# Performance work log

Hardware: AMD Instinct MI355X
Metric: run time of the kernel (lower is better)

The kernel has to match this reference:

```python
import jax, jax.numpy as jnp
import numpy as np

B, G = 256, 24
N = B * G
D_IN, HEADS, D_HEAD = 128, 8, 64  # out_channels = in_channels//2 = 64, concat=False
EFF = HEADS * D_HEAD
EPS = 1e-5
SCALE = float(np.sqrt(D_HEAD))

def _gelu(x):
    return jax.nn.gelu(x, approximate=False)

def _pff(x, w1, b1, w2, b2):
    # PositionwiseFeedForward, dropout=0 (eval)
    return _gelu(x @ w1.T + b1) @ w2.T + b2

def _graph_norm_global(x, w, b, ms):
    # GraphNorm called without batch -> single graph over all N nodes
    mean = jnp.mean(x, axis=0, keepdims=True)
    out = x - mean * ms
    var = jnp.mean(out * out, axis=0, keepdims=True)
    return w * out / jnp.sqrt(var + EPS) + b

def _graph_norm(x, w, b, ms, batch, nseg):
    cnt = jax.ops.segment_sum(jnp.ones((x.shape[0],), x.dtype), batch, nseg)[:, None]
    mean = jax.ops.segment_sum(x, batch, nseg) / cnt
    out = x - mean[batch] * ms
    var = jax.ops.segment_sum(out * out, batch, nseg) / cnt
    return w * out / jnp.sqrt(var + EPS)[batch] + b

def _segment_softmax(logits, seg, nseg):
    m = jax.ops.segment_max(logits, seg, num_segments=nseg)
    e = jnp.exp(logits - m[seg])
    s = jax.ops.segment_sum(e, seg, num_segments=nseg)
    return e / (s[seg] + 1e-16)

def _attn_conv(x, edge_index, p):
    (nq_w, nq_b, nq_ms, wq, bq, wk, bk, wv, bv,
     no_w, no_b, no_ms, o_w1, o_b1, o_w2, o_b2) = p
    n = x.shape[0]
    xin = x
    xn = _graph_norm_global(x, nq_w, nq_b, nq_ms)
    q = (xn @ wq.T + bq).reshape(n, HEADS, D_HEAD)
    k = (xn @ wk.T + bk).reshape(n, HEADS, D_HEAD)
    v = (xn @ wv.T + bv).reshape(n, HEADS, D_HEAD)
    loops = jnp.arange(n, dtype=edge_index.dtype)  # add_self_loops appends
    src = jnp.concatenate([edge_index[0], loops])
    dst = jnp.concatenate([edge_index[1], loops])
    qk = jnp.sum(q[dst] * k[src], axis=-1) / SCALE          # [E', H]
    alpha = _segment_softmax(qk, dst, n)                     # segment softmax over dst
    aggr = jax.ops.segment_sum(v[src] * alpha[:, :, None], dst, num_segments=n)  # [N,H,Dh]
    aggr = aggr.mean(axis=1)                                 # concat=False: head mean -> [N,64]
    init = xin.reshape(n, D_IN // D_HEAD, D_HEAD).sum(axis=1)  # sum-fold 128 -> 64 residual
    h = aggr + init
    hn = _graph_norm_global(h, no_w, no_b, no_ms)
    return h + _pff(hn, o_w1, o_b1, o_w2, o_b2)


def setup_inputs() -> dict:
    key = jax.random.key(0)
    ks = jax.random.split(key, 12)
    # block-dense edges: fully connected within each set, no self loops
    a = np.arange(G)
    ii, jj = np.meshgrid(a, a, indexing='ij')
    m = ii != jj
    dst_l, src_l = ii[m], jj[m]
    offs = (np.arange(B) * G)[:, None]
    src = (src_l[None, :] + offs).reshape(-1)
    dst = (dst_l[None, :] + offs).reshape(-1)
    edge_index = jnp.asarray(np.stack([src, dst]), dtype=jnp.int64)
    batch = jnp.asarray(np.repeat(np.arange(B), G), dtype=jnp.int64)
    ptr = jnp.asarray(np.arange(B + 1) * G, dtype=jnp.int64)
    x = jax.random.normal(ks[0], (N, D_IN), jnp.float32)
    def lin(k, o, i):
        return jax.random.normal(k, (o, i), jnp.float32) * (1.0 / np.sqrt(i))
    d = dict(x=x, edge_index=edge_index, ptr=ptr, batch=batch)
    d.update(nq_w=jnp.ones((D_IN,)), nq_b=jnp.zeros((D_IN,)), nq_ms=jnp.ones((D_IN,)))
    d.update(wq=lin(ks[1], EFF, D_IN), bq=jnp.zeros((EFF,)),
             wk=lin(ks[2], EFF, D_IN), bk=jnp.zeros((EFF,)),
             wv=lin(ks[3], EFF, D_IN), bv=jnp.zeros((EFF,)))
    d.update(no_w=jnp.ones((D_HEAD,)), no_b=jnp.zeros((D_HEAD,)), no_ms=jnp.ones((D_HEAD,)))
    d.update(o_w1=lin(ks[4], D_HEAD, D_HEAD), o_b1=jnp.zeros((D_HEAD,)),
             o_w2=lin(ks[5], D_HEAD, D_HEAD), o_b2=jnp.zeros((D_HEAD,)))
    d.update(pn_w=jnp.ones((D_HEAD,)), pn_b=jnp.zeros((D_HEAD,)), pn_ms=jnp.ones((D_HEAD,)))
    d.update(p_w1=lin(ks[6], D_HEAD, D_HEAD), p_b1=jnp.zeros((D_HEAD,)),
             p_w2=lin(ks[7], 1, D_HEAD), p_b2=jnp.zeros((1,)))
    return d


def reference(x, edge_index, ptr, batch,
              nq_w, nq_b, nq_ms, wq, bq, wk, bk, wv, bv,
              no_w, no_b, no_ms, o_w1, o_b1, o_w2, o_b2,
              pn_w, pn_b, pn_ms, p_w1, p_b1, p_w2, p_b2):
    nseg = ptr.shape[0] - 1
    h = _attn_conv(x, edge_index,
                   (nq_w, nq_b, nq_ms, wq, bq, wk, bk, wv, bv,
                    no_w, no_b, no_ms, o_w1, o_b1, o_w2, o_b2))   # [N,64]
    hn = _graph_norm(h, pn_w, pn_b, pn_ms, batch, nseg)
    score = _pff(hn, p_w1, p_b1, p_w2, p_b2)                       # [N,1]
    w = _segment_softmax(score[:, 0], batch, nseg)[:, None]        # per-set softmax
    return jax.ops.segment_sum(x * w, batch, num_segments=nseg)    # [B, 128]
```

## Files before the change

kernel.cpp:

```cpp
#include <hip/hip_runtime.h>
#include <stdint.h>


#define N_NODES 6144
#define GSIZE 24
#define NGRAPH 256
#define DIN 128
#define DH 64
#define EFF 512
#define EPSN 1e-5f

typedef __attribute__((ext_vector_type(8))) __bf16 bf16x8;
typedef __attribute__((ext_vector_type(4))) float f32x4;
union U16B { uint4 u; bf16x8 v; unsigned short s[8]; };

__device__ inline unsigned short f2bf(float f){
  unsigned u = __float_as_uint(f);
  u += 0x7fff + ((u>>16)&1);
  return (unsigned short)(u>>16);
}
__device__ inline float gelu_exact(float x){ return 0.5f*x*(1.0f+erff(x*0.70710678118654752f)); }

#define XS    0
#define HS    256
#define WT1   81920
#define WT2   86016
#define PWT1  90112
#define FBo   94208
#define WCVT_BYTE  385024
#define HCOMB_BYTE 778240

#define QSTRIDE 516

__global__ __launch_bounds__(256)
void k_pre(const float* __restrict__ x,
           const float* __restrict__ o_w1, const float* __restrict__ o_w2,
           const float* __restrict__ p_w1,
           const float* __restrict__ o_b1, const float* __restrict__ o_b2,
           const float* __restrict__ p_b1, const float* __restrict__ p_w2,
           const float* __restrict__ p_b2,
           const float* __restrict__ wq, const float* __restrict__ wk,
           const float* __restrict__ wv,
           float* __restrict__ wsf){
  int t = threadIdx.x;
  int bi = blockIdx.x;
  if(bi < 192){
    int c = t & 127, h = t >> 7;
    float s = 0.f, q = 0.f;
    #pragma unroll
    for(int r = 0; r < 16; ++r){
      float v = x[(size_t)(bi*32 + h + 2*r)*DIN + c];
      s += v; q += v*v;
    }
    __shared__ float sm[256], sm2[256];
    sm[t] = s; sm2[t] = q;
    __syncthreads();
    if(t < 128){
      atomicAdd(&wsf[XS + t],       sm[t] + sm[t+128]);
      atomicAdd(&wsf[XS + 128 + t], sm2[t] + sm2[t+128]);
    }
    return;
  }
  if(bi < 195){
    const float* src; float* dst;
    if(bi == 192){ src = o_w1; dst = wsf + WT1; }
    else if(bi == 193){ src = o_w2; dst = wsf + WT2; }
    else { src = p_w1; dst = wsf + PWT1; }
    for(int p = t; p < DH*DH; p += 256){
      int r = p >> 6, c = p & 63;
      dst[c*DH + r] = src[p];
    }
    if(bi == 192){
      float* fb = wsf + FBo;
      if(t < 64){
        fb[t]       = o_b1[t];
        fb[64 + t]  = o_b2[t];
        fb[128 + t] = p_b1[t];
        fb[192 + t] = p_w2[t];
      }
      if(t == 0) fb[256] = p_b2[0];
    }
    return;
  }
  int j = bi - 195;
  int mat = j >> 2, seg = j & 3;
  const float* src = (mat==0) ? wq : (mat==1) ? wk : wv;
  unsigned short* dst = (unsigned short*)((char*)wsf + WCVT_BYTE)
                        + (size_t)mat*EFF*DIN + seg*16384;
  const float* sp = src + seg*16384;
  for(int e = t*8; e < 16384; e += 2048){
    float4 a = *(const float4*)(sp + e);
    float4 b = *(const float4*)(sp + e + 4);
    U16B o;
    o.s[0]=f2bf(a.x); o.s[1]=f2bf(a.y); o.s[2]=f2bf(a.z); o.s[3]=f2bf(a.w);
    o.s[4]=f2bf(b.x); o.s[5]=f2bf(b.y); o.s[6]=f2bf(b.z); o.s[7]=f2bf(b.w);
    *(uint4*)(dst + e) = o.u;
  }
}

#define LOADW(nt, W, B) do{ \
  const int mat_ = (nt)>>2, sub_ = (nt)&3; \
  const unsigned short* wp_ = wcvt + (size_t)mat_*EFF*DIN \
      + (size_t)(h*64 + sub_*16 + m)*DIN + lq*8; \
  W[0] = *(const uint4*)(wp_);      W[1] = *(const uint4*)(wp_ + 32); \
  W[2] = *(const uint4*)(wp_ + 64); W[3] = *(const uint4*)(wp_ + 96); \
  const float* bias_ = (mat_==0) ? bq : (mat_==1) ? bk : bv; \
  B = *(const float4*)(bias_ + h*64 + sub_*16 + lq*4); \
}while(0)

#define COMPW(nt, W, B) do{ \
  const int mat_ = (nt)>>2, sub_ = (nt)&3; \
  f32x4 a0_ = {0.f,0.f,0.f,0.f}, a1_ = {0.f,0.f,0.f,0.f}; \
  U16B w8_; \
  w8_.u = W[0]; \
  a0_ = __builtin_amdgcn_mfma_f32_16x16x32_bf16(w8_.v, afr[0][0], a0_, 0, 0, 0); \
  a1_ = __builtin_amdgcn_mfma_f32_16x16x32_bf16(w8_.v, afr[1][0], a1_, 0, 0, 0); \
  w8_.u = W[1]; \
  a0_ = __builtin_amdgcn_mfma_f32_16x16x32_bf16(w8_.v, afr[0][1], a0_, 0, 0, 0); \
  a1_ = __builtin_amdgcn_mfma_f32_16x16x32_bf16(w8_.v, afr[1][1], a1_, 0, 0, 0); \
  w8_.u = W[2]; \
  a0_ = __builtin_amdgcn_mfma_f32_16x16x32_bf16(w8_.v, afr[0][2], a0_, 0, 0, 0); \
  a1_ = __builtin_amdgcn_mfma_f32_16x16x32_bf16(w8_.v, afr[1][2], a1_, 0, 0, 0); \
  w8_.u = W[3]; \
  a0_ = __builtin_amdgcn_mfma_f32_16x16x32_bf16(w8_.v, afr[0][3], a0_, 0, 0, 0); \
  a1_ = __builtin_amdgcn_mfma_f32_16x16x32_bf16(w8_.v, afr[1][3], a1_, 0, 0, 0); \
  float* dst_ = qlds + mat_*(GSIZE*QSTRIDE); \
  const int col_ = h*64 + sub_*16 + lq*4; \
  { float4 o_; o_.x=a0_[0]+B.x; o_.y=a0_[1]+B.y; o_.z=a0_[2]+B.z; o_.w=a0_[3]+B.w; \
    *(float4*)(dst_ + m*QSTRIDE + col_) = o_; } \
  if(m < 8){ float4 o_; o_.x=a1_[0]+B.x; o_.y=a1_[1]+B.y; o_.z=a1_[2]+B.z; o_.w=a1_[3]+B.w; \
    *(float4*)(dst_ + (16+m)*QSTRIDE + col_) = o_; } \
}while(0)

__global__ __launch_bounds__(512)
void k_attn2(const float* __restrict__ x,
             const float* __restrict__ bq, const float* __restrict__ bk,
             const float* __restrict__ bv,
             const float* __restrict__ nq_w, const float* __restrict__ nq_b,
             const float* __restrict__ nq_ms,
             float* __restrict__ ws, float* __restrict__ hcomb){
  __shared__ __align__(16) float qlds[3*GSIZE*QSTRIDE];
  __shared__ __align__(16) float hv[GSIZE][68];
  __shared__ float A1s[DIN], C1s[DIN];

  int t = threadIdx.x, g = blockIdx.x, base = g*GSIZE;
  int h = t >> 6, l = t & 63;
  const unsigned short* wcvt = (const unsigned short*)((const char*)ws + WCVT_BYTE);

  for(int i = t; i < GSIZE*68; i += 512) ((float*)hv)[i] = 0.f;

  if(t < 128){
    float s1 = ws[XS + t];
    float q1 = ws[XS + 128 + t];
    float mean = s1 * (1.0f / N_NODES);
    float ex2  = q1 * (1.0f / N_NODES);
    float cm   = mean * nq_ms[t];
    float var  = ex2 - 2.f*cm*mean + cm*cm;
    float rstd = rsqrtf(var + EPSN);
    float a    = nq_w[t] * rstd;
    A1s[t] = a; C1s[t] = nq_b[t] - a*cm;
  }
  __syncthreads();

  int m = l & 15, lq = l >> 4;

  bf16x8 afr[2][4];
  #pragma unroll
  for(int mt = 0; mt < 2; ++mt){
    int row = mt*16 + m; if(row > GSIZE-1) row = GSIZE-1;
    const float* xr = x + (size_t)(base + row)*DIN;
    #pragma unroll
    for(int kk = 0; kk < 4; ++kk){
      int k0 = kk*32 + lq*8;
      float4 a = *(const float4*)(xr + k0);
      float4 b = *(const float4*)(xr + k0 + 4);
      U16B u;
      u.s[0] = f2bf(a.x*A1s[k0+0] + C1s[k0+0]);
      u.s[1] = f2bf(a.y*A1s[k0+1] + C1s[k0+1]);
      u.s[2] = f2bf(a.z*A1s[k0+2] + C1s[k0+2]);
      u.s[3] = f2bf(a.w*A1s[k0+3] + C1s[k0+3]);
      u.s[4] = f2bf(b.x*A1s[k0+4] + C1s[k0+4]);
      u.s[5] = f2bf(b.y*A1s[k0+5] + C1s[k0+5]);
      u.s[6] = f2bf(b.z*A1s[k0+6] + C1s[k0+6]);
      u.s[7] = f2bf(b.w*A1s[k0+7] + C1s[k0+7]);
      afr[mt][kk] = u.v;
    }
  }

  {
    uint4 wA[4], wB[4], wC[4];
    float4 bA, bB, bC;
    LOADW(0, wA, bA);  LOADW(1, wB, bB);
    LOADW(2, wC, bC);  COMPW(0, wA, bA);
    LOADW(3, wA, bA);  COMPW(1, wB, bB);
    LOADW(4, wB, bB);  COMPW(2, wC, bC);
    LOADW(5, wC, bC);  COMPW(3, wA, bA);
    LOADW(6, wA, bA);  COMPW(4, wB, bB);
    LOADW(7, wB, bB);  COMPW(5, wC, bC);
    LOADW(8, wC, bC);  COMPW(6, wA, bA);
    LOADW(9, wA, bA);  COMPW(7, wB, bB);
    LOADW(10, wB, bB); COMPW(8, wC, bC);
    LOADW(11, wC, bC); COMPW(9, wA, bA);
    COMPW(10, wB, bB);
    COMPW(11, wC, bC);
  }

  {
    int r0 = 3*(l >> 3), j0 = 3*(l & 7);
    const float* qp = qlds + r0*QSTRIDE + h*64;
    const float* kp = qlds + GSIZE*QSTRIDE + j0*QSTRIDE + h*64;
    float s00=0.f,s01=0.f,s02=0.f,s10=0.f,s11=0.f,s12=0.f,s20=0.f,s21=0.f,s22=0.f;
    #pragma unroll
    for(int d4 = 0; d4 < 16; ++d4){
      float4 q0 = *(const float4*)(qp + d4*4);
      float4 q1 = *(const float4*)(qp + QSTRIDE + d4*4);
      float4 q2 = *(const float4*)(qp + 2*QSTRIDE + d4*4);
      float4 k0 = *(const float4*)(kp + d4*4);
      float4 k1 = *(const float4*)(kp + QSTRIDE + d4*4);
      float4 k2 = *(const float4*)(kp + 2*QSTRIDE + d4*4);
      s00 += q0.x*k0.x + q0.y*k0.y + q0.z*k0.z + q0.w*k0.w;
      s01 += q0.x*k1.x + q0.y*k1.y + q0.z*k1.z + q0.w*k1.w;
      s02 += q0.x*k2.x + q0.y*k2.y + q0.z*k2.z + q0.w*k2.w;
      s10 += q1.x*k0.x + q1.y*k0.y + q1.z*k0.z + q1.w*k0.w;
      s11 += q1.x*k1.x + q1.y*k1.y + q1.z*k1.z + q1.w*k1.w;
      s12 += q1.x*k2.x + q1.y*k2.y + q1.z*k2.z + q1.w*k2.w;
      s20 += q2.x*k0.x + q2.y*k0.y + q2.z*k0.z + q2.w*k0.w;
      s21 += q2.x*k1.x + q2.y*k1.y + q2.z*k1.z + q2.w*k1.w;
      s22 += q2.x*k2.x + q2.y*k2.y + q2.z*k2.z + q2.w*k2.w;
    }
    float a0, a1, a2, m0, su, inv;
    float* STb = qlds + h*64;
    a0 = s00*0.125f; a1 = s01*0.125f; a2 = s02*0.125f;
    m0 = fmaxf(fmaxf(a0, a1), a2);
    #pragma unroll
    for(int o = 1; o < 8; o <<= 1) m0 = fmaxf(m0, __shfl_xor(m0, o, 8));
    a0 = __expf(a0-m0); a1 = __expf(a1-m0); a2 = __expf(a2-m0);
    su = a0 + a1 + a2;
    #pragma unroll
    for(int o = 1; o < 8; o <<= 1) su += __shfl_xor(su, o, 8);
    inv = 1.0f/(su + 1e-16f);
    STb[(j0+0)*QSTRIDE + r0] = a0*inv; STb[(j0+1)*QSTRIDE + r0] = a1*inv; STb[(j0+2)*QSTRIDE + r0] = a2*inv;
    a0 = s10*0.125f; a1 = s11*0.125f; a2 = s12*0.125f;
    m0 = fmaxf(fmaxf(a0, a1), a2);
    #pragma unroll
    for(int o = 1; o < 8; o <<= 1) m0 = fmaxf(m0, __shfl_xor(m0, o, 8));
    a0 = __expf(a0-m0); a1 = __expf(a1-m0); a2 = __expf(a2-m0);
    su = a0 + a1 + a2;
    #pragma unroll
    for(int o = 1; o < 8; o <<= 1) su += __shfl_xor(su, o, 8);
    inv = 1.0f/(su + 1e-16f);
    STb[(j0+0)*QSTRIDE + r0+1] = a0*inv; STb[(j0+1)*QSTRIDE + r0+1] = a1*inv; STb[(j0+2)*QSTRIDE + r0+1] = a2*inv;
    a0 = s20*0.125f; a1 = s21*0.125f; a2 = s22*0.125f;
    m0 = fmaxf(fmaxf(a0, a1), a2);
    #pragma unroll
    for(int o = 1; o < 8; o <<= 1) m0 = fmaxf(m0, __shfl_xor(m0, o, 8));
    a0 = __expf(a0-m0); a1 = __expf(a1-m0); a2 = __expf(a2-m0);
    su = a0 + a1 + a2;
    #pragma unroll
    for(int o = 1; o < 8; o <<= 1) su += __shfl_xor(su, o, 8);
    inv = 1.0f/(su + 1e-16f);
    STb[(j0+0)*QSTRIDE + r0+2] = a0*inv; STb[(j0+1)*QSTRIDE + r0+2] = a1*inv; STb[(j0+2)*QSTRIDE + r0+2] = a2*inv;
  }

  {
    float o24[GSIZE];
    #pragma unroll
    for(int r = 0; r < GSIZE; ++r) o24[r] = 0.f;
    const float* vp  = qlds + 2*GSIZE*QSTRIDE + h*64 + l;
    const float* STb = qlds + h*64;
    #pragma unroll
    for(int j = 0; j < GSIZE; ++j){
      float v = vp[j*QSTRIDE];
      #pragma unroll
      for(int rq = 0; rq < 6; ++rq){
        float4 p4 = *(const float4*)(STb + j*QSTRIDE + rq*4);
        o24[rq*4+0] = fmaf(p4.x, v, o24[rq*4+0]);
        o24[rq*4+1] = fmaf(p4.y, v, o24[rq*4+1]);
        o24[rq*4+2] = fmaf(p4.z, v, o24[rq*4+2]);
        o24[rq*4+3] = fmaf(p4.w, v, o24[rq*4+3]);
      }
    }
    #pragma unroll
    for(int r = 0; r < GSIZE; ++r) atomicAdd(&hv[r][l], o24[r]);
  }
  __syncthreads();

  #pragma unroll
  for(int sl = 0; sl < 3; ++sl){
    int idx = t + sl*512;
    int r = idx >> 6, d = idx & 63;
    const float* xr = x + (size_t)(base + r)*DIN;
    float hval = hv[r][d]*0.125f + xr[d] + xr[64 + d];
    hcomb[(size_t)(base + r)*DH + d] = hval;
    hv[r][d] = hval;
  }
  __syncthreads();
  if(t < 64){
    float s1 = 0.f, s2 = 0.f;
    #pragma unroll
    for(int i = 0; i < GSIZE; ++i){ float v = hv[i][t]; s1 += v; s2 += v*v; }
    atomicAdd(&ws[HS + t],      s1);
    atomicAdd(&ws[HS + 64 + t], s2);
  }
}

__global__ __launch_bounds__(512)
void k_final(const float* __restrict__ x,
             const float* __restrict__ hbuf, const float* __restrict__ ws,
             const float* __restrict__ no_w, const float* __restrict__ no_b,
             const float* __restrict__ no_ms,
             const float* __restrict__ pn_w, const float* __restrict__ pn_b,
             const float* __restrict__ pn_ms,
             float* __restrict__ out){
  __shared__ __align__(16) float W1[4096];
  __shared__ __align__(16) float W2[4096];
  __shared__ __align__(16) float PW1[4096];
  __shared__ __align__(16) float fbs[260];
  __shared__ __align__(16) float hs[GSIZE][68];
  __shared__ __align__(16) float hn[GSIZE][68];
  __shared__ __align__(16) float ts[GSIZE][68];
  __shared__ float A2s[DH], C2s[DH];
  __shared__ float a3[DH], c3[DH];
  __shared__ float scores[GSIZE], wsm[GSIZE];

  int t = threadIdx.x;
  int base = blockIdx.x * GSIZE;
  int c = t & 63, i0 = t >> 6;

  {
    const float4* s1 = (const float4*)(ws + WT1);
    const float4* s2 = (const float4*)(ws + WT2);
    const float4* s3 = (const float4*)(ws + PWT1);
    #pragma unroll
    for(int it = 0; it < 2; ++it){
      int i = t + it*512;
      ((float4*)W1)[i]  = s1[i];
      ((float4*)W2)[i]  = s2[i];
      ((float4*)PW1)[i] = s3[i];
    }
    if(t < 257) fbs[t] = ws[FBo + t];
    if(t < DH){
      float a1 = ws[HS + t];
      float a2 = ws[HS + 64 + t];
      float mean = a1 * (1.0f / N_NODES);
      float ex2  = a2 * (1.0f / N_NODES);
      float cm   = mean * no_ms[t];
      float var  = ex2 - 2.f*cm*mean + cm*cm;
      float rstd = rsqrtf(var + EPSN);
      float a    = no_w[t] * rstd;
      A2s[t] = a; C2s[t] = no_b[t] - a*cm;
    }
  }
  __syncthreads();
  {
    float a2 = A2s[c];
    float c2 = C2s[c];
    #pragma unroll
    for(int r = 0; r < 3; ++r){
      int i = i0 + 8*r;
      float hvv = hbuf[(size_t)(base + i)*DH + c];
      hs[i][c] = hvv;
      hn[i][c] = a2*hvv + c2;
    }
  }
  __syncthreads();

  {
    float acc[3];
    #pragma unroll
    for(int r = 0; r < 3; ++r) acc[r] = fbs[c];
    #pragma unroll 16
    for(int k = 0; k < DH; ++k){
      float w = W1[k*DH + c];
      #pragma unroll
      for(int r = 0; r < 3; ++r) acc[r] = fmaf(hn[i0 + 8*r][k], w, acc[r]);
    }
    #pragma unroll
    for(int r = 0; r < 3; ++r) ts[i0 + 8*r][c] = gelu_exact(acc[r]);
  }
  __syncthreads();

  {
    float acc[3];
    #pragma unroll
    for(int r = 0; r < 3; ++r) acc[r] = fbs[64 + c];
    #pragma unroll 16
    for(int k = 0; k < DH; ++k){
      float w = W2[k*DH + c];
      #pragma unroll
      for(int r = 0; r < 3; ++r) acc[r] = fmaf(ts[i0 + 8*r][k], w, acc[r]);
    }
    #pragma unroll
    for(int r = 0; r < 3; ++r) hs[i0 + 8*r][c] += acc[r];
  }
  __syncthreads();

  if(t < DH){
    float s1 = 0.f, s2 = 0.f;
    #pragma unroll
    for(int i = 0; i < GSIZE; i++){ float v = hs[i][t]; s1 += v; s2 += v*v; }
    float mean = s1 * (1.0f / GSIZE);
    float ex2  = s2 * (1.0f / GSIZE);
    float cm   = mean * pn_ms[t];
    float var  = ex2 - 2.f*cm*mean + cm*cm;
    float rstd = rsqrtf(var + EPSN);
    float a    = pn_w[t] * rstd;
    a3[t] = a; c3[t] = pn_b[t] - a*cm;
  }
  __syncthreads();

  {
    float acc[3];
    #pragma unroll
    for(int r = 0; r < 3; ++r) acc[r] = fbs[128 + c];
    #pragma unroll 16
    for(int k = 0; k < DH; ++k){
      float w  = PW1[k*DH + c];
      float ak = a3[k], ck = c3[k];
      #pragma unroll
      for(int r = 0; r < 3; ++r){
        float hnv = fmaf(ak, hs[i0 + 8*r][k], ck);
        acc[r] = fmaf(hnv, w, acc[r]);
      }
    }
    #pragma unroll
    for(int r = 0; r < 3; ++r) ts[i0 + 8*r][c] = gelu_exact(acc[r]);
  }
  __syncthreads();

  if(t < GSIZE){
    const float4* tp = (const float4*)ts[t];
    const float4* wp = (const float4*)(fbs + 192);
    float s = fbs[256];
    #pragma unroll
    for(int q = 0; q < 16; ++q){
      float4 a = tp[q], b = wp[q];
      s += a.x*b.x + a.y*b.y + a.z*b.z + a.w*b.w;
    }
    scores[t] = s;
  }
  __syncthreads();
  if(t < GSIZE){
    float mx = -1e30f;
    #pragma unroll
    for(int j = 0; j < GSIZE; j++) mx = fmaxf(mx, scores[j]);
    float sum = 0.f;
    #pragma unroll
    for(int j = 0; j < GSIZE; j++) sum += __expf(scores[j] - mx);
    wsm[t] = __expf(scores[t] - mx) / (sum + 1e-16f);
  }
  __syncthreads();
  if(t < DIN){
    float s = 0.f;
    #pragma unroll 8
    for(int i = 0; i < GSIZE; i++) s += wsm[i] * x[(size_t)(base+i)*DIN + t];
    out[(size_t)blockIdx.x*DIN + t] = s;
  }
}

extern "C" void kernel_launch(void* const* d_in, const int* in_sizes, int n_in,
                              void* d_out, int out_size, void* d_ws, size_t ws_size,
                              hipStream_t stream){
  (void)in_sizes; (void)n_in; (void)out_size; (void)ws_size;
  const float* x    = (const float*)d_in[0];
  const float* nq_w = (const float*)d_in[4];
  const float* nq_b = (const float*)d_in[5];
  const float* nq_ms= (const float*)d_in[6];
  const float* wq   = (const float*)d_in[7];
  const float* bq   = (const float*)d_in[8];
  const float* wk   = (const float*)d_in[9];
  const float* bk   = (const float*)d_in[10];
  const float* wv   = (const float*)d_in[11];
  const float* bv   = (const float*)d_in[12];
  const float* no_w = (const float*)d_in[13];
  const float* no_b = (const float*)d_in[14];
  const float* no_ms= (const float*)d_in[15];
  const float* o_w1 = (const float*)d_in[16];
  const float* o_b1 = (const float*)d_in[17];
  const float* o_w2 = (const float*)d_in[18];
  const float* o_b2 = (const float*)d_in[19];
  const float* pn_w = (const float*)d_in[20];
  const float* pn_b = (const float*)d_in[21];
  const float* pn_ms= (const float*)d_in[22];
  const float* p_w1 = (const float*)d_in[23];
  const float* p_b1 = (const float*)d_in[24];
  const float* p_w2 = (const float*)d_in[25];
  const float* p_b2 = (const float*)d_in[26];

  float* ws    = (float*)d_ws;
  float* hcomb = (float*)((char*)d_ws + HCOMB_BYTE);

  hipMemsetAsync(d_ws, 0, 384*sizeof(float), stream);
  k_pre<<<207, 256, 0, stream>>>(x, o_w1, o_w2, p_w1, o_b1, o_b2, p_b1, p_w2, p_b2,
                                 wq, wk, wv, ws);
  k_attn2<<<NGRAPH, 512, 0, stream>>>(x, bq, bk, bv, nq_w, nq_b, nq_ms, ws, hcomb);
  k_final<<<NGRAPH, 512, 0, stream>>>(x, hcomb, ws, no_w, no_b, no_ms,
                                      pn_w, pn_b, pn_ms, (float*)d_out);
}
```

Baseline: 167.0 us.

## Split attention across two blocks per graph by head halves, add residual fixup kernel

The attention kernel now launches two blocks per graph, each handling four heads, with two waves per head splitting the QKV output tiles, the dot-product dimension and the output rows. Partial head sums go into a zeroed hcomb buffer through global atomics. A new small kernel then adds the folded input residual and accumulates the GraphNorm statistics. The aim is more parallelism and smaller per-block shared memory, at the cost of an extra launch, a larger memset, global atomics and more block barriers.

Result: slower. 176.1 us (+5.4%).

```diff
diff --git a/kernel.cpp b/kernel.cpp
--- a/kernel.cpp
+++ b/kernel.cpp
@@ -23,14 +23,14 @@
 
 #define XS    0
 #define HS    256
-#define WT1   81920
-#define WT2   86016
-#define PWT1  90112
-#define FBo   94208
-#define WCVT_BYTE  385024
-#define HCOMB_BYTE 778240
-
-#define QSTRIDE 516
+#define HCF   384
+#define WT1   393600
+#define WT2   397696
+#define PWT1  401792
+#define FBo   405888
+#define WCVT_BYTE  1703936
+
+#define QS3 260
 
 __global__ __launch_bounds__(256)
 void k_pre(const float* __restrict__ x,
@@ -98,17 +98,17 @@
   }
 }
 
-#define LOADW(nt, W, B) do{ \
+#define LOADW3(nt, W, B) do{ \
   const int mat_ = (nt)>>2, sub_ = (nt)&3; \
   const unsigned short* wp_ = wcvt + (size_t)mat_*EFF*DIN \
-      + (size_t)(h*64 + sub_*16 + m)*DIN + lq*8; \
+      + (size_t)(gh*64 + sub_*16 + m)*DIN + lq*8; \
   W[0] = *(const uint4*)(wp_);      W[1] = *(const uint4*)(wp_ + 32); \
   W[2] = *(const uint4*)(wp_ + 64); W[3] = *(const uint4*)(wp_ + 96); \
   const float* bias_ = (mat_==0) ? bq : (mat_==1) ? bk : bv; \
-  B = *(const float4*)(bias_ + h*64 + sub_*16 + lq*4); \
+  B = *(const float4*)(bias_ + gh*64 + sub_*16 + lq*4); \
 }while(0)
 
-#define COMPW(nt, W, B) do{ \
+#define COMPW3(nt, W, B) do{ \
   const int mat_ = (nt)>>2, sub_ = (nt)&3; \
   f32x4 a0_ = {0.f,0.f,0.f,0.f}, a1_ = {0.f,0.f,0.f,0.f}; \
   U16B w8_; \
@@ -124,30 +124,34 @@
   w8_.u = W[3]; \
   a0_ = __builtin_amdgcn_mfma_f32_16x16x32_bf16(w8_.v, afr[0][3], a0_, 0, 0, 0); \
   a1_ = __builtin_amdgcn_mfma_f32_16x16x32_bf16(w8_.v, afr[1][3], a1_, 0, 0, 0); \
-  float* dst_ = qlds + mat_*(GSIZE*QSTRIDE); \
-  const int col_ = h*64 + sub_*16 + lq*4; \
+  float* dst_ = qlds + mat_*(GSIZE*QS3); \
+  const int col_ = hh*64 + sub_*16 + lq*4; \
   { float4 o_; o_.x=a0_[0]+B.x; o_.y=a0_[1]+B.y; o_.z=a0_[2]+B.z; o_.w=a0_[3]+B.w; \
-    *(float4*)(dst_ + m*QSTRIDE + col_) = o_; } \
+    *(float4*)(dst_ + m*QS3 + col_) = o_; } \
   if(m < 8){ float4 o_; o_.x=a1_[0]+B.x; o_.y=a1_[1]+B.y; o_.z=a1_[2]+B.z; o_.w=a1_[3]+B.w; \
-    *(float4*)(dst_ + (16+m)*QSTRIDE + col_) = o_; } \
+    *(float4*)(dst_ + (16+m)*QS3 + col_) = o_; } \
 }while(0)
 
 __global__ __launch_bounds__(512)
-void k_attn2(const float* __restrict__ x,
+void k_attn3(const float* __restrict__ x,
              const float* __restrict__ bq, const float* __restrict__ bk,
              const float* __restrict__ bv,
              const float* __restrict__ nq_w, const float* __restrict__ nq_b,
              const float* __restrict__ nq_ms,
              float* __restrict__ ws, float* __restrict__ hcomb){
-  __shared__ __align__(16) float qlds[3*GSIZE*QSTRIDE];
-  __shared__ __align__(16) float hv[GSIZE][68];
-  __shared__ float A1s[DIN], C1s[DIN];
-
-  int t = threadIdx.x, g = blockIdx.x, base = g*GSIZE;
-  int h = t >> 6, l = t & 63;
+  __shared__ __align__(16) float qlds[3*GSIZE*QS3];
+  __shared__ __align__(16) float hv[GSIZE][DH];
+  float* A1s = qlds;
+  float* C1s = qlds + 128;
+
+  int t = threadIdx.x, b = blockIdx.x;
+  int base = (b >> 1)*GSIZE;
+  int w = t >> 6, l = t & 63;
+  int hh = w >> 1, half = w & 1;
+  int gh = (b & 1)*4 + hh;
   const unsigned short* wcvt = (const unsigned short*)((const char*)ws + WCVT_BYTE);
 
-  for(int i = t; i < GSIZE*68; i += 512) ((float*)hv)[i] = 0.f;
+  for(int i = t; i < GSIZE*DH; i += 512) ((float*)hv)[i] = 0.f;
 
   if(t < 128){
     float s1 = ws[XS + t];
@@ -186,38 +190,36 @@
       afr[mt][kk] = u.v;
     }
   }
+  __syncthreads();
 
   {
     uint4 wA[4], wB[4], wC[4];
     float4 bA, bB, bC;
-    LOADW(0, wA, bA);  LOADW(1, wB, bB);
-    LOADW(2, wC, bC);  COMPW(0, wA, bA);
-    LOADW(3, wA, bA);  COMPW(1, wB, bB);
-    LOADW(4, wB, bB);  COMPW(2, wC, bC);
-    LOADW(5, wC, bC);  COMPW(3, wA, bA);
-    LOADW(6, wA, bA);  COMPW(4, wB, bB);
-    LOADW(7, wB, bB);  COMPW(5, wC, bC);
-    LOADW(8, wC, bC);  COMPW(6, wA, bA);
-    LOADW(9, wA, bA);  COMPW(7, wB, bB);
-    LOADW(10, wB, bB); COMPW(8, wC, bC);
-    LOADW(11, wC, bC); COMPW(9, wA, bA);
-    COMPW(10, wB, bB);
-    COMPW(11, wC, bC);
-  }
-
-  {
-    int r0 = 3*(l >> 3), j0 = 3*(l & 7);
-    const float* qp = qlds + r0*QSTRIDE + h*64;
-    const float* kp = qlds + GSIZE*QSTRIDE + j0*QSTRIDE + h*64;
-    float s00=0.f,s01=0.f,s02=0.f,s10=0.f,s11=0.f,s12=0.f,s20=0.f,s21=0.f,s22=0.f;
-    #pragma unroll
-    for(int d4 = 0; d4 < 16; ++d4){
+    int nb = half*6;
+    LOADW3(nb+0, wA, bA);  LOADW3(nb+1, wB, bB);
+    LOADW3(nb+2, wC, bC);  COMPW3(nb+0, wA, bA);
+    LOADW3(nb+3, wA, bA);  COMPW3(nb+1, wB, bB);
+    LOADW3(nb+4, wB, bB);  COMPW3(nb+2, wC, bC);
+    LOADW3(nb+5, wC, bC);  COMPW3(nb+3, wA, bA);
+    COMPW3(nb+4, wB, bB);
+    COMPW3(nb+5, wC, bC);
+  }
+  __syncthreads();
+
+  int r0 = half*12 + 3*(l >> 4), j0 = 3*(l & 7);
+  float s00=0.f,s01=0.f,s02=0.f,s10=0.f,s11=0.f,s12=0.f,s20=0.f,s21=0.f,s22=0.f;
+  {
+    int d8 = (l >> 3) & 1;
+    const float* qp = qlds + r0*QS3 + hh*64 + d8*32;
+    const float* kp = qlds + GSIZE*QS3 + j0*QS3 + hh*64 + d8*32;
+    #pragma unroll
+    for(int d4 = 0; d4 < 8; ++d4){
       float4 q0 = *(const float4*)(qp + d4*4);
-      float4 q1 = *(const float4*)(qp + QSTRIDE + d4*4);
-      float4 q2 = *(const float4*)(qp + 2*QSTRIDE + d4*4);
+      float4 q1 = *(const float4*)(qp + QS3 + d4*4);
+      float4 q2 = *(const float4*)(qp + 2*QS3 + d4*4);
       float4 k0 = *(const float4*)(kp + d4*4);
-      float4 k1 = *(const float4*)(kp + QSTRIDE + d4*4);
-      float4 k2 = *(const float4*)(kp + 2*QSTRIDE + d4*4);
+      float4 k1 = *(const float4*)(kp + QS3 + d4*4);
+      float4 k2 = *(const float4*)(kp + 2*QS3 + d4*4);
       s00 += q0.x*k0.x + q0.y*k0.y + q0.z*k0.z + q0.w*k0.w;
       s01 += q0.x*k1.x + q0.y*k1.y + q0.z*k1.z + q0.w*k1.w;
       s02 += q0.x*k2.x + q0.y*k2.y + q0.z*k2.z + q0.w*k2.w;
@@ -228,8 +230,15 @@
       s21 += q2.x*k1.x + q2.y*k1.y + q2.z*k1.z + q2.w*k1.w;
       s22 += q2.x*k2.x + q2.y*k2.y + q2.z*k2.z + q2.w*k2.w;
     }
+    s00 += __shfl_xor(s00, 8); s01 += __shfl_xor(s01, 8); s02 += __shfl_xor(s02, 8);
+    s10 += __shfl_xor(s10, 8); s11 += __shfl_xor(s11, 8); s12 += __shfl_xor(s12, 8);
+    s20 += __shfl_xor(s20, 8); s21 += __shfl_xor(s21, 8); s22 += __shfl_xor(s22, 8);
+  }
+  __syncthreads();
+
+  {
     float a0, a1, a2, m0, su, inv;
-    float* STb = qlds + h*64;
+    float* STb = qlds + hh*64;
     a0 = s00*0.125f; a1 = s01*0.125f; a2 = s02*0.125f;
     m0 = fmaxf(fmaxf(a0, a1), a2);
     #pragma unroll
@@ -239,7 +248,7 @@
     #pragma unroll
     for(int o = 1; o < 8; o <<= 1) su += __shfl_xor(su, o, 8);
     inv = 1.0f/(su + 1e-16f);
-    STb[(j0+0)*QSTRIDE + r0] = a0*inv; STb[(j0+1)*QSTRIDE + r0] = a1*inv; STb[(j0+2)*QSTRIDE + r0] = a2*inv;
+    STb[(j0+0)*QS3 + r0] = a0*inv; STb[(j0+1)*QS3 + r0] = a1*inv; STb[(j0+2)*QS3 + r0] = a2*inv;
     a0 = s10*0.125f; a1 = s11*0.125f; a2 = s12*0.125f;
     m0 = fmaxf(fmaxf(a0, a1), a2);
     #pragma unroll
@@ -249,7 +258,7 @@
     #pragma unroll
     for(int o = 1; o < 8; o <<= 1) su += __shfl_xor(su, o, 8);
     inv = 1.0f/(su + 1e-16f);
-    STb[(j0+0)*QSTRIDE + r0+1] = a0*inv; STb[(j0+1)*QSTRIDE + r0+1] = a1*inv; STb[(j0+2)*QSTRIDE + r0+1] = a2*inv;
+    STb[(j0+0)*QS3 + r0+1] = a0*inv; STb[(j0+1)*QS3 + r0+1] = a1*inv; STb[(j0+2)*QS3 + r0+1] = a2*inv;
     a0 = s20*0.125f; a1 = s21*0.125f; a2 = s22*0.125f;
     m0 = fmaxf(fmaxf(a0, a1), a2);
     #pragma unroll
@@ -259,29 +268,31 @@
     #pragma unroll
     for(int o = 1; o < 8; o <<= 1) su += __shfl_xor(su, o, 8);
     inv = 1.0f/(su + 1e-16f);
-    STb[(j0+0)*QSTRIDE + r0+2] = a0*inv; STb[(j0+1)*QSTRIDE + r0+2] = a1*inv; STb[(j0+2)*QSTRIDE + r0+2] = a2*inv;
-  }
-
-  {
-    float o24[GSIZE];
-    #pragma unroll
-    for(int r = 0; r < GSIZE; ++r) o24[r] = 0.f;
-    const float* vp  = qlds + 2*GSIZE*QSTRIDE + h*64 + l;
-    const float* STb = qlds + h*64;
+    STb[(j0+0)*QS3 + r0+2] = a0*inv; STb[(j0+1)*QS3 + r0+2] = a1*inv; STb[(j0+2)*QS3 + r0+2] = a2*inv;
+  }
+  __syncthreads();
+
+  {
+    float o12[12];
+    #pragma unroll
+    for(int r = 0; r < 12; ++r) o12[r] = 0.f;
+    const float* vp  = qlds + 2*GSIZE*QS3 + hh*64 + l;
+    const float* STb = qlds + hh*64;
+    int rb = half*12;
     #pragma unroll
     for(int j = 0; j < GSIZE; ++j){
-      float v = vp[j*QSTRIDE];
+      float v = vp[j*QS3];
       #pragma unroll
-      for(int rq = 0; rq < 6; ++rq){
-        float4 p4 = *(const float4*)(STb + j*QSTRIDE + rq*4);
-        o24[rq*4+0] = fmaf(p4.x, v, o24[rq*4+0]);
-        o24[rq*4+1] = fmaf(p4.y, v, o24[rq*4+1]);
-        o24[rq*4+2] = fmaf(p4.z, v, o24[rq*4+2]);
-        o24[rq*4+3] = fmaf(p4.w, v, o24[rq*4+3]);
+      for(int rq = 0; rq < 3; ++rq){
+        float4 p4 = *(const float4*)(STb + j*QS3 + rb + rq*4);
+        o12[rq*4+0] = fmaf(p4.x, v, o12[rq*4+0]);
+        o12[rq*4+1] = fmaf(p4.y, v, o12[rq*4+1]);
+        o12[rq*4+2] = fmaf(p4.z, v, o12[rq*4+2]);
+        o12[rq*4+3] = fmaf(p4.w, v, o12[rq*4+3]);
       }
     }
     #pragma unroll
-    for(int r = 0; r < GSIZE; ++r) atomicAdd(&hv[r][l], o24[r]);
+    for(int r = 0; r < 12; ++r) atomicAdd(&hv[rb + r][l], o12[r]);
   }
   __syncthreads();
 
@@ -289,18 +300,33 @@
   for(int sl = 0; sl < 3; ++sl){
     int idx = t + sl*512;
     int r = idx >> 6, d = idx & 63;
-    const float* xr = x + (size_t)(base + r)*DIN;
-    float hval = hv[r][d]*0.125f + xr[d] + xr[64 + d];
-    hcomb[(size_t)(base + r)*DH + d] = hval;
-    hv[r][d] = hval;
-  }
+    atomicAdd(&hcomb[(size_t)(base + r)*DH + d], hv[r][d]*0.125f);
+  }
+}
+
+__global__ __launch_bounds__(256)
+void k_hfix(const float* __restrict__ x, float* __restrict__ ws,
+            float* __restrict__ hcomb){
+  __shared__ float redA[256], redB[256];
+  int t = threadIdx.x, b = blockIdx.x;
+  int d = t & 63, rg = t >> 6;
+  int r0 = b*32 + rg*8;
+  float s1 = 0.f, s2 = 0.f;
+  #pragma unroll
+  for(int k = 0; k < 8; ++k){
+    int r = r0 + k;
+    const float* xr = x + (size_t)r*DIN;
+    float v = hcomb[(size_t)r*DH + d] + xr[d] + xr[64 + d];
+    hcomb[(size_t)r*DH + d] = v;
+    s1 += v; s2 += v*v;
+  }
+  redA[t] = s1; redB[t] = s2;
   __syncthreads();
   if(t < 64){
-    float s1 = 0.f, s2 = 0.f;
-    #pragma unroll
-    for(int i = 0; i < GSIZE; ++i){ float v = hv[i][t]; s1 += v; s2 += v*v; }
-    atomicAdd(&ws[HS + t],      s1);
-    atomicAdd(&ws[HS + 64 + t], s2);
+    float a1 = redA[t] + redA[t+64] + redA[t+128] + redA[t+192];
+    float a2 = redB[t] + redB[t+64] + redB[t+128] + redB[t+192];
+    atomicAdd(&ws[HS + t],      a1);
+    atomicAdd(&ws[HS + 64 + t], a2);
   }
 }
 
@@ -488,12 +514,13 @@
   const float* p_b2 = (const float*)d_in[26];
 
   float* ws    = (float*)d_ws;
-  float* hcomb = (float*)((char*)d_ws + HCOMB_BYTE);
-
-  hipMemsetAsync(d_ws, 0, 384*sizeof(float), stream);
+  float* hcomb = ws + HCF;
+
+  hipMemsetAsync(d_ws, 0, (size_t)(384 + N_NODES*DH)*sizeof(float), stream);
   k_pre<<<207, 256, 0, stream>>>(x, o_w1, o_w2, p_w1, o_b1, o_b2, p_b1, p_w2, p_b2,
                                  wq, wk, wv, ws);
-  k_attn2<<<NGRAPH, 512, 0, stream>>>(x, bq, bk, bv, nq_w, nq_b, nq_ms, ws, hcomb);
+  k_attn3<<<512, 512, 0, stream>>>(x, bq, bk, bv, nq_w, nq_b, nq_ms, ws, hcomb);
+  k_hfix<<<192, 256, 0, stream>>>(x, ws, hcomb);
   k_final<<<NGRAPH, 512, 0, stream>>>(x, hcomb, ws, no_w, no_b, no_ms,
                                       pn_w, pn_b, pn_ms, (float*)d_out);
 }
```
